# Performance work log

Hardware: AMD Instinct MI355X
Metric: run time of the kernel (lower is better)

Reference implementation:

```python
import jax, jax.numpy as jnp
import numpy as np

N_NODES = 100000
N_EDGES = 3200000
IN_DIM = 256
HID = 64


def setup_inputs() -> dict:
    key = jax.random.key(0)
    ks = jax.random.split(key, 8)
    x = jax.random.normal(ks[0], (N_NODES, IN_DIM), dtype=jnp.float32)
    edge_index = jax.random.randint(ks[1], (2, N_EDGES), 0, N_NODES, dtype=jnp.int32)
    s = lambda k, shp, fan_in: jax.random.normal(k, shp, dtype=jnp.float32) / np.sqrt(fan_in)
    return {
        "x": x,
        "edge_index": edge_index,
        "W1": s(ks[2], (IN_DIM, HID), IN_DIM),
        "b1": jnp.zeros((HID,), jnp.float32),
        "W2": s(ks[3], (HID, HID), HID),
        "b2": jnp.zeros((HID,), jnp.float32),
        "Wl1": s(ks[4], (2 * HID, HID), 2 * HID),
        "bl1": jnp.zeros((HID,), jnp.float32),
        "Wl2": s(ks[5], (HID, 1), HID),
        "bl2": jnp.zeros((1,), jnp.float32),
    }


def gcn_conv(h, src, dst, W, b, n_nodes):
    # PyG GCNConv: linear transform, add self-loops, symmetric norm, scatter-add
    h = h @ W  # [N, out]
    loop = jnp.arange(n_nodes, dtype=src.dtype)
    src_f = jnp.concatenate([src, loop])
    dst_f = jnp.concatenate([dst, loop])
    deg = jax.ops.segment_sum(jnp.ones_like(dst_f, dtype=h.dtype), dst_f,
                              num_segments=n_nodes)
    dinv = jnp.where(deg > 0, jax.lax.rsqrt(jnp.maximum(deg, 1e-12)), 0.0)
    norm = dinv[src_f] * dinv[dst_f]  # [E+N]
    msg = h[src_f] * norm[:, None]     # gather + scale
    out = jax.ops.segment_sum(msg, dst_f, num_segments=n_nodes)
    return out + b


def reference(x, edge_index, W1, b1, W2, b2, Wl1, bl1, Wl2, bl2):
    n = x.shape[0]
    src, dst = edge_index[0], edge_index[1]
    # encode (inference: dropout is identity)
    h = gcn_conv(x, src, dst, W1, b1, n)
    h = jax.nn.relu(h)
    z = gcn_conv(h, src, dst, W2, b2, n)
    # decode: gather src/dst embeddings, concat, MLP, sigmoid
    ef = jnp.concatenate([z[src], z[dst]], axis=1)  # [E, 2*HID]
    e = jax.nn.relu(ef @ Wl1 + bl1)
    e = e @ Wl2 + bl2
    return jax.nn.sigmoid(e)
```

## Files before the change

kernel.cpp:

```cpp
#include <hip/hip_runtime.h>
#include <hip/hip_bf16.h>
#include <math.h>

#define HID 64
#define IN_DIM 256
#define NPB 400
#define NB  250
#define CAP 14336
#define TILE 8192
#define NW  64
#define NKEY (NPB * NW)

typedef unsigned short u16;
typedef unsigned int u32;

using bf16x8 = __attribute__((ext_vector_type(8))) short;
using f32x4  = __attribute__((ext_vector_type(4))) float;

__device__ __forceinline__ float bf2f(u16 v) {
    return __uint_as_float((u32)v << 16);
}
__device__ __forceinline__ u16 f2bf(float f) {
    __hip_bfloat16 b = __float2bfloat16(f);
    return *(u16*)&b;
}

__global__ __launch_bounds__(256) void binit(int* __restrict__ bcur) {
    int b = threadIdx.x + blockIdx.x * 256;
    if (b < NB) bcur[b] = b * CAP;
}

__global__ __launch_bounds__(256) void bucket_fill(const int* __restrict__ src,
                                                   const int* __restrict__ dst,
                                                   int* __restrict__ bcur,
                                                   int2* __restrict__ bpair, int E) {
    __shared__ int hist[NB], cnt2[NB], gbase[NB];
    int tid = threadIdx.x;
    int base = blockIdx.x * TILE;
    for (int i = tid; i < NB; i += 256) { hist[i] = 0; cnt2[i] = 0; }
    __syncthreads();
    for (int i = 0; i < TILE / 256; ++i) {
        int e = base + i * 256 + tid;
        if (e < E) atomicAdd(&hist[dst[e] / NPB], 1);
    }
    __syncthreads();
    for (int b = tid; b < NB; b += 256)
        if (hist[b]) gbase[b] = atomicAdd(&bcur[b], hist[b]);
    __syncthreads();
    for (int i = 0; i < TILE / 256; ++i) {
        int e = base + i * 256 + tid;
        if (e < E) {
            int d = dst[e];
            int b = d / NPB;
            int lp = atomicAdd(&cnt2[b], 1);
            bpair[gbase[b] + lp] = make_int2(src[e], ((d - b * NPB) << 22) | e);
        }
    }
}

__global__ __launch_bounds__(512) void csr_scatter(const int* __restrict__ bcur,
                                                   const int2* __restrict__ bpair,
                                                   int* __restrict__ csr_src,
                                                   int* __restrict__ csr_eid,
                                                   int* __restrict__ noff,
                                                   int* __restrict__ ndeg,
                                                   float* __restrict__ dinv) {
    extern __shared__ int smem[];
    int* cnt  = smem;
    int* tsum = smem + NKEY;
    int* wsum = smem + NKEY + 512;
    int tid = threadIdx.x, b = blockIdx.x;
    int node0 = b * NPB;
    int pbeg = b * CAP;
    int cntE = bcur[b] - pbeg;

    for (int i = tid; i < NKEY; i += 512) cnt[i] = 0;
    __syncthreads();
    for (int i = tid; i < cntE; i += 512) {
        int2 p = bpair[pbeg + i];
        int key = (((p.y >> 22) & 511) << 6) | ((u32)p.x >> 11);
        atomicAdd(&cnt[key], 1);
    }
    __syncthreads();
    {
        int base = tid * (NKEY / 512);
        int s = 0;
#pragma unroll
        for (int j = 0; j < NKEY / 512; ++j) s += cnt[base + j];
        tsum[tid] = s;
    }
    __syncthreads();
    {
        int lane = tid & 63, wid = tid >> 6;
        int v = tsum[tid];
        int incl = v;
#pragma unroll
        for (int s = 1; s < 64; s <<= 1) {
            int t = __shfl_up(incl, s, 64);
            if (lane >= s) incl += t;
        }
        if (lane == 63) wsum[wid] = incl;
        __syncthreads();
        if (tid == 0) {
            int run = 0;
#pragma unroll
            for (int w = 0; w < 8; ++w) { int t = wsum[w]; wsum[w] = run; run += t; }
        }
        __syncthreads();
        tsum[tid] = wsum[wid] + incl - v;
    }
    __syncthreads();
    {
        int base = tid * (NKEY / 512);
        int run = tsum[tid];
#pragma unroll
        for (int j = 0; j < NKEY / 512; ++j) {
            int cv = cnt[base + j];
            cnt[base + j] = run;
            run += cv;
        }
    }
    __syncthreads();
    for (int dl = tid; dl < NPB; dl += 512) {
        int beg = cnt[dl << 6];
        int end = (dl < NPB - 1) ? cnt[(dl + 1) << 6] : cntE;
        noff[node0 + dl] = pbeg + beg;
        ndeg[node0 + dl] = end - beg;
        dinv[node0 + dl] = rsqrtf((float)(end - beg) + 1.0f);
    }
    __syncthreads();
    for (int i = tid; i < cntE; i += 512) {
        int2 p = bpair[pbeg + i];
        int key = (((p.y >> 22) & 511) << 6) | ((u32)p.x >> 11);
        int pos = atomicAdd(&cnt[key], 1);
        csr_src[pbeg + pos] = p.x;
        csr_eid[pbeg + pos] = p.y & 0x3FFFFF;
    }
}

template<int K, int COLS, int MODE>
__global__ __launch_bounds__(256) void mfma_gemm(const float* __restrict__ A,
                                                 const float* __restrict__ W,
                                                 const float* __restrict__ dinv,
                                                 const float* __restrict__ bias,
                                                 u16* __restrict__ out_b,
                                                 float* __restrict__ out_f,
                                                 int N) {
    constexpr int KP = K + 8;
    constexpr int NT = COLS / 16;
    __shared__ __align__(16) u16 Wh[COLS * KP];
    __shared__ __align__(16) u16 Wl[COLS * KP];

    const int tid  = threadIdx.x;
    const int wave = tid >> 6;
    const int lane = tid & 63;
    const int lr   = lane & 15;
    const int kg   = lane >> 4;
    const int row0 = blockIdx.x * 64;

    for (int e = tid; e < K * COLS; e += 256) {
        int k = e / COLS, c = e % COLS;
        int gidx = (MODE == 2) ? (((c >> 6) * K + k) * 64 + (c & 63)) : e;
        float f = W[gidx];
        u16 hi = f2bf(f);
        u16 lo = f2bf(f - bf2f(hi));
        Wh[c * KP + k] = hi;
        Wl[c * KP + k] = lo;
    }
    __syncthreads();

    const int arow = row0 + wave * 16 + lr;
    const float* ar = A + (size_t)(arow < N ? arow : N - 1) * K + kg * 8;

    f32x4 acc[NT];
#pragma unroll
    for (int c = 0; c < NT; ++c) acc[c] = (f32x4){0.f, 0.f, 0.f, 0.f};

#pragma unroll
    for (int ks = 0; ks < K; ks += 32) {
        float4 v0 = *(const float4*)(ar + ks);
        float4 v1 = *(const float4*)(ar + ks + 4);
        bf16x8 ah, al;
        {
            u16 h0 = f2bf(v0.x), h1 = f2bf(v0.y), h2 = f2bf(v0.z), h3 = f2bf(v0.w);
            u16 h4 = f2bf(v1.x), h5 = f2bf(v1.y), h6 = f2bf(v1.z), h7 = f2bf(v1.w);
            ah = (bf16x8){(short)h0, (short)h1, (short)h2, (short)h3,
                          (short)h4, (short)h5, (short)h6, (short)h7};
            al = (bf16x8){(short)f2bf(v0.x - bf2f(h0)), (short)f2bf(v0.y - bf2f(h1)),
                          (short)f2bf(v0.z - bf2f(h2)), (short)f2bf(v0.w - bf2f(h3)),
                          (short)f2bf(v1.x - bf2f(h4)), (short)f2bf(v1.y - bf2f(h5)),
                          (short)f2bf(v1.z - bf2f(h6)), (short)f2bf(v1.w - bf2f(h7))};
        }
#pragma unroll
        for (int c = 0; c < NT; ++c) {
            const int wrow = c * 16 + lr;
            bf16x8 bh = *(const bf16x8*)(Wh + wrow * KP + ks + kg * 8);
            bf16x8 bl = *(const bf16x8*)(Wl + wrow * KP + ks + kg * 8);
            acc[c] = __builtin_amdgcn_mfma_f32_16x16x32_bf16(ah, bh, acc[c], 0, 0, 0);
            acc[c] = __builtin_amdgcn_mfma_f32_16x16x32_bf16(ah, bl, acc[c], 0, 0, 0);
            acc[c] = __builtin_amdgcn_mfma_f32_16x16x32_bf16(al, bh, acc[c], 0, 0, 0);
        }
    }

#pragma unroll
    for (int rr = 0; rr < 4; ++rr) {
        int n = row0 + wave * 16 + kg * 4 + rr;
        if (n >= N) continue;
        float dv = (MODE == 0) ? dinv[n] : 1.f;
#pragma unroll
        for (int c = 0; c < NT; ++c) {
            int col = c * 16 + lr;
            float v = acc[c][rr];
            if (MODE == 0) {
                out_b[(size_t)n * 64 + col] = f2bf(v * dv);
            } else {
                if (col < 64) out_b[(size_t)n * 64 + col] = f2bf(v);
                else out_f[(size_t)n * 64 + (col - 64)] = v + bias[col - 64];
            }
        }
    }
}

__global__ __launch_bounds__(256) void gather_kernel(const int* __restrict__ noff,
                                                     const int* __restrict__ ndeg,
                                                     const int* __restrict__ csr_src,
                                                     const u16* __restrict__ ts,
                                                     const float* __restrict__ dinv,
                                                     const float* __restrict__ bias,
                                                     float* __restrict__ outh, int N,
                                                     int do_relu) {
    long tid = (long)blockIdx.x * blockDim.x + threadIdx.x;
    int v = (int)(tid >> 6), j = (int)(tid & 63);
    if (v >= N) return;
    int l = j & 7, g = j >> 3;
    const uint4* tp = (const uint4*)ts;
    float a0 = 0.f, a1 = 0.f, a2 = 0.f, a3 = 0.f;
    float a4 = 0.f, a5 = 0.f, a6 = 0.f, a7 = 0.f;
    int beg = noff[v], end = beg + ndeg[v];

#define ACCUM(U)                              \
    a0 += __uint_as_float((U).x << 16);       \
    a1 += __uint_as_float((U).x & 0xffff0000u); \
    a2 += __uint_as_float((U).y << 16);       \
    a3 += __uint_as_float((U).y & 0xffff0000u); \
    a4 += __uint_as_float((U).z << 16);       \
    a5 += __uint_as_float((U).z & 0xffff0000u); \
    a6 += __uint_as_float((U).w << 16);       \
    a7 += __uint_as_float((U).w & 0xffff0000u);

    int k = beg + g;
    while (k + 24 < end) {
        int s0 = csr_src[k];
        int s1 = csr_src[k + 8];
        int s2 = csr_src[k + 16];
        int s3 = csr_src[k + 24];
        uint4 u0 = tp[((u32)s0 << 3) + l];
        uint4 u1 = tp[((u32)s1 << 3) + l];
        uint4 u2 = tp[((u32)s2 << 3) + l];
        uint4 u3 = tp[((u32)s3 << 3) + l];
        ACCUM(u0); ACCUM(u1); ACCUM(u2); ACCUM(u3);
        k += 32;
    }
    while (k < end) {
        int s = csr_src[k];
        uint4 u = tp[((u32)s << 3) + l];
        ACCUM(u);
        k += 8;
    }
#pragma unroll
    for (int o = 8; o < 64; o <<= 1) {
        a0 += __shfl_xor(a0, o, 64);
        a1 += __shfl_xor(a1, o, 64);
        a2 += __shfl_xor(a2, o, 64);
        a3 += __shfl_xor(a3, o, 64);
        a4 += __shfl_xor(a4, o, 64);
        a5 += __shfl_xor(a5, o, 64);
        a6 += __shfl_xor(a6, o, 64);
        a7 += __shfl_xor(a7, o, 64);
    }
    uint4 su = tp[((u32)v << 3) + l];
    ACCUM(su);
#undef ACCUM
    float dv = dinv[v];
    const float* bp = bias + 8 * l;
    float4 b4a = *(const float4*)(bp);
    float4 b4b = *(const float4*)(bp + 4);
    float4 r0, r1;
    r0.x = a0 * dv + b4a.x; r0.y = a1 * dv + b4a.y;
    r0.z = a2 * dv + b4a.z; r0.w = a3 * dv + b4a.w;
    r1.x = a4 * dv + b4b.x; r1.y = a5 * dv + b4b.y;
    r1.z = a6 * dv + b4b.z; r1.w = a7 * dv + b4b.w;
    if (do_relu) {
        r0.x = fmaxf(r0.x, 0.f); r0.y = fmaxf(r0.y, 0.f);
        r0.z = fmaxf(r0.z, 0.f); r0.w = fmaxf(r0.w, 0.f);
        r1.x = fmaxf(r1.x, 0.f); r1.y = fmaxf(r1.y, 0.f);
        r1.z = fmaxf(r1.z, 0.f); r1.w = fmaxf(r1.w, 0.f);
    }
    if (g == 0) {
        float* op = outh + ((u32)v << 6) + 8 * l;
        *(float4*)(op) = r0;
        *(float4*)(op + 4) = r1;
    }
}

__global__ __launch_bounds__(256) void decode_kernel(const int* __restrict__ noff,
                                                     const int* __restrict__ ndeg,
                                                     const int* __restrict__ csr_src,
                                                     const int* __restrict__ csr_eid,
                                                     const u16* __restrict__ a,
                                                     const float* __restrict__ c,
                                                     const float* __restrict__ Wl2,
                                                     const float* __restrict__ bl2,
                                                     float* __restrict__ out, int N) {
    long tid = (long)blockIdx.x * blockDim.x + threadIdx.x;
    int v = (int)(tid >> 6), j = (int)(tid & 63);
    if (v >= N) return;
    int l = j & 7, g = j >> 3;
    const float* cv = c + ((u32)v << 6) + 8 * l;
    float4 ca = *(const float4*)(cv);
    float4 cb = *(const float4*)(cv + 4);
    const float* wv = Wl2 + 8 * l;
    float4 wa = *(const float4*)(wv);
    float4 wb = *(const float4*)(wv + 4);
    float bl2v = bl2[0];
    const uint4* ap = (const uint4*)a;
    int beg = noff[v], end = beg + ndeg[v];

#define EDGEP(U, P)                                                   \
    {                                                                 \
        float f0 = __uint_as_float((U).x << 16);                      \
        float f1 = __uint_as_float((U).x & 0xffff0000u);              \
        float f2 = __uint_as_float((U).y << 16);                      \
        float f3 = __uint_as_float((U).y & 0xffff0000u);              \
        float f4 = __uint_as_float((U).z << 16);                      \
        float f5 = __uint_as_float((U).z & 0xffff0000u);              \
        float f6 = __uint_as_float((U).w << 16);                      \
        float f7 = __uint_as_float((U).w & 0xffff0000u);              \
        P  = fmaxf(f0 + ca.x, 0.f) * wa.x;                            \
        P += fmaxf(f1 + ca.y, 0.f) * wa.y;                            \
        P += fmaxf(f2 + ca.z, 0.f) * wa.z;                            \
        P += fmaxf(f3 + ca.w, 0.f) * wa.w;                            \
        P += fmaxf(f4 + cb.x, 0.f) * wb.x;                            \
        P += fmaxf(f5 + cb.y, 0.f) * wb.y;                            \
        P += fmaxf(f6 + cb.z, 0.f) * wb.z;                            \
        P += fmaxf(f7 + cb.w, 0.f) * wb.w;                            \
    }

    int k = beg + g;
    while (k + 8 < end) {
        int s0 = csr_src[k];
        int s1 = csr_src[k + 8];
        int e0 = csr_eid[k];
        int e1 = csr_eid[k + 8];
        uint4 u0 = ap[((u32)s0 << 3) + l];
        uint4 u1 = ap[((u32)s1 << 3) + l];
        float p0, p1;
        EDGEP(u0, p0);
        EDGEP(u1, p1);
        p0 += __shfl_xor(p0, 1, 64);
        p1 += __shfl_xor(p1, 1, 64);
        p0 += __shfl_xor(p0, 2, 64);
        p1 += __shfl_xor(p1, 2, 64);
        p0 += __shfl_xor(p0, 4, 64);
        p1 += __shfl_xor(p1, 4, 64);
        if (l == 0) {
            out[e0] = __builtin_amdgcn_rcpf(1.f + __expf(-(p0 + bl2v)));
            out[e1] = __builtin_amdgcn_rcpf(1.f + __expf(-(p1 + bl2v)));
        }
        k += 16;
    }
    if (k < end) {
        int s0 = csr_src[k];
        int e0 = csr_eid[k];
        uint4 u0 = ap[((u32)s0 << 3) + l];
        float p0;
        EDGEP(u0, p0);
        p0 += __shfl_xor(p0, 1, 64);
        p0 += __shfl_xor(p0, 2, 64);
        p0 += __shfl_xor(p0, 4, 64);
        if (l == 0) out[e0] = __builtin_amdgcn_rcpf(1.f + __expf(-(p0 + bl2v)));
    }
#undef EDGEP
}

extern "C" void kernel_launch(void* const* d_in, const int* in_sizes, int n_in,
                              void* d_out, int out_size, void* d_ws, size_t ws_size,
                              hipStream_t stream) {
    const float* x   = (const float*)d_in[0];
    const int*   ei  = (const int*)d_in[1];
    const float* W1  = (const float*)d_in[2];
    const float* b1  = (const float*)d_in[3];
    const float* W2  = (const float*)d_in[4];
    const float* b2  = (const float*)d_in[5];
    const float* Wl1 = (const float*)d_in[6];
    const float* bl1 = (const float*)d_in[7];
    const float* Wl2 = (const float*)d_in[8];
    const float* bl2 = (const float*)d_in[9];
    float* out = (float*)d_out;

    const int N = in_sizes[0] / IN_DIM;
    const int E = in_sizes[1] / 2;
    const int* src = ei;
    const int* dst = ei + E;

    char* ws = (char*)d_ws;
    float* dinv    = (float*)ws;  ws += (size_t)(N + 64) * 4;
    int*   noff    = (int*)ws;    ws += (size_t)(N + 64) * 4;
    int*   ndeg    = (int*)ws;    ws += (size_t)(N + 64) * 4;
    int*   bcur    = (int*)ws;    ws += 1024;
    int*   csr_src = (int*)ws;    ws += (size_t)NB * CAP * 4;
    int*   csr_eid = (int*)ws;    ws += (size_t)NB * CAP * 4;
    u16*   tb      = (u16*)ws;    ws += (size_t)N * HID * 2;
    float* h       = (float*)ws;  ws += (size_t)N * HID * 4;
    float* c       = (float*)ws;  ws += (size_t)N * HID * 4;
    int2*  bpair   = (int2*)h;

    const int TPB = 256;
    long nodeT = (long)N * HID;
    int nodeBlocks = (int)((nodeT + TPB - 1) / TPB);
    int tBlocks = (E + TILE - 1) / TILE;
    int gBlocks = (N + 63) / 64;
    size_t sortBytes = (size_t)(NKEY + 512 + 8) * sizeof(int);

    binit<<<1, TPB, 0, stream>>>(bcur);
    bucket_fill<<<tBlocks, TPB, 0, stream>>>(src, dst, bcur, bpair, E);
    csr_scatter<<<NB, 512, sortBytes, stream>>>(bcur, bpair, csr_src, csr_eid,
                                                noff, ndeg, dinv);

    mfma_gemm<IN_DIM, 64, 0><<<gBlocks, TPB, 0, stream>>>(x, W1, dinv, nullptr, tb, nullptr, N);
    gather_kernel<<<nodeBlocks, TPB, 0, stream>>>(noff, ndeg, csr_src, tb, dinv, b1, h, N, 1);

    mfma_gemm<HID, 64, 0><<<gBlocks, TPB, 0, stream>>>(h, W2, dinv, nullptr, tb, nullptr, N);
    gather_kernel<<<nodeBlocks, TPB, 0, stream>>>(noff, ndeg, csr_src, tb, dinv, b2, h, N, 0);

    mfma_gemm<HID, 128, 2><<<gBlocks, TPB, 0, stream>>>(h, Wl1, nullptr, bl1, tb, c, N);

    decode_kernel<<<nodeBlocks, TPB, 0, stream>>>(noff, ndeg, csr_src, csr_eid, tb, c, Wl2, bl2, out, N);
}
```

Before: 423.8 us.

## Bucket decode outputs by edge id and scatter through LDS for coalesced writes

The decode kernel no longer writes each sigmoid output straight to a random edge position. Results are staged as (edge id, value) pairs in LDS and binned into edge-id buckets with atomics, then a new oscatter kernel assembles each bucket in shared memory and writes it out with coalesced float4 stores. Each block now handles 16 nodes per wave, so there are fewer blocks. This removes uncoalesced 4-byte scattered stores to the output, at the cost of an extra kernel pass, 8-byte pair traffic, LDS/global atomics, and reuse of the h buffer as pair storage.

```diff
diff --git a/kernel.cpp b/kernel.cpp
--- a/kernel.cpp
+++ b/kernel.cpp
@@ -10,6 +10,8 @@
 #define TILE 8192
 #define NW  64
 #define NKEY (NPB * NW)
+#define OEB 12800
+#define LCAP 2560
 
 typedef unsigned short u16;
 typedef unsigned int u32;
@@ -25,9 +27,13 @@
     return *(u16*)&b;
 }
 
-__global__ __launch_bounds__(256) void binit(int* __restrict__ bcur) {
+__global__ __launch_bounds__(256) void binit(int* __restrict__ bcur,
+                                             int* __restrict__ ocur) {
     int b = threadIdx.x + blockIdx.x * 256;
-    if (b < NB) bcur[b] = b * CAP;
+    if (b < NB) {
+        bcur[b] = b * CAP;
+        ocur[b] = b * OEB;
+    }
 }
 
 __global__ __launch_bounds__(256) void bucket_fill(const int* __restrict__ src,
@@ -311,20 +317,37 @@
                                                      const float* __restrict__ c,
                                                      const float* __restrict__ Wl2,
                                                      const float* __restrict__ bl2,
-                                                     float* __restrict__ out, int N) {
-    long tid = (long)blockIdx.x * blockDim.x + threadIdx.x;
-    int v = (int)(tid >> 6), j = (int)(tid & 63);
-    if (v >= N) return;
+                                                     int2* __restrict__ opair,
+                                                     int* __restrict__ ocur, int N) {
+    __shared__ int2 lbuf[LCAP];
+    __shared__ int lhist[NB];
+    __shared__ int lgb[NB];
+    __shared__ int lcnt;
+    int tid = threadIdx.x;
+    for (int i = tid; i < NB; i += 256) lhist[i] = 0;
+    if (tid == 0) lcnt = 0;
+    __syncthreads();
+
+    int wave = tid >> 6, j = tid & 63;
     int l = j & 7, g = j >> 3;
-    const float* cv = c + ((u32)v << 6) + 8 * l;
-    float4 ca = *(const float4*)(cv);
-    float4 cb = *(const float4*)(cv + 4);
     const float* wv = Wl2 + 8 * l;
     float4 wa = *(const float4*)(wv);
     float4 wb = *(const float4*)(wv + 4);
     float bl2v = bl2[0];
     const uint4* ap = (const uint4*)a;
-    int beg = noff[v], end = beg + ndeg[v];
+    int node0 = blockIdx.x * 64 + wave * 16;
+
+#define EMIT(EID, VAL)                                                       \
+    {                                                                        \
+        int idx_ = atomicAdd(&lcnt, 1);                                      \
+        if (idx_ < LCAP) {                                                   \
+            lbuf[idx_] = make_int2((EID), __float_as_int(VAL));              \
+            atomicAdd(&lhist[(EID) / OEB], 1);                               \
+        } else {                                                             \
+            int pos_ = atomicAdd(&ocur[(EID) / OEB], 1);                     \
+            opair[pos_] = make_int2((EID), __float_as_int(VAL));             \
+        }                                                                    \
+    }
 
 #define EDGEP(U, P)                                                   \
     {                                                                 \
@@ -346,41 +369,89 @@
         P += fmaxf(f7 + cb.w, 0.f) * wb.w;                            \
     }
 
-    int k = beg + g;
-    while (k + 8 < end) {
-        int s0 = csr_src[k];
-        int s1 = csr_src[k + 8];
-        int e0 = csr_eid[k];
-        int e1 = csr_eid[k + 8];
-        uint4 u0 = ap[((u32)s0 << 3) + l];
-        uint4 u1 = ap[((u32)s1 << 3) + l];
-        float p0, p1;
-        EDGEP(u0, p0);
-        EDGEP(u1, p1);
-        p0 += __shfl_xor(p0, 1, 64);
-        p1 += __shfl_xor(p1, 1, 64);
-        p0 += __shfl_xor(p0, 2, 64);
-        p1 += __shfl_xor(p1, 2, 64);
-        p0 += __shfl_xor(p0, 4, 64);
-        p1 += __shfl_xor(p1, 4, 64);
-        if (l == 0) {
-            out[e0] = __builtin_amdgcn_rcpf(1.f + __expf(-(p0 + bl2v)));
-            out[e1] = __builtin_amdgcn_rcpf(1.f + __expf(-(p1 + bl2v)));
-        }
-        k += 16;
-    }
-    if (k < end) {
-        int s0 = csr_src[k];
-        int e0 = csr_eid[k];
-        uint4 u0 = ap[((u32)s0 << 3) + l];
-        float p0;
-        EDGEP(u0, p0);
-        p0 += __shfl_xor(p0, 1, 64);
-        p0 += __shfl_xor(p0, 2, 64);
-        p0 += __shfl_xor(p0, 4, 64);
-        if (l == 0) out[e0] = __builtin_amdgcn_rcpf(1.f + __expf(-(p0 + bl2v)));
+    for (int ni = 0; ni < 16; ++ni) {
+        int v = node0 + ni;
+        if (v >= N) break;
+        const float* cv = c + ((u32)v << 6) + 8 * l;
+        float4 ca = *(const float4*)(cv);
+        float4 cb = *(const float4*)(cv + 4);
+        int beg = noff[v], end = beg + ndeg[v];
+
+        int k = beg + g;
+        while (k + 8 < end) {
+            int s0 = csr_src[k];
+            int s1 = csr_src[k + 8];
+            int e0 = csr_eid[k];
+            int e1 = csr_eid[k + 8];
+            uint4 u0 = ap[((u32)s0 << 3) + l];
+            uint4 u1 = ap[((u32)s1 << 3) + l];
+            float p0, p1;
+            EDGEP(u0, p0);
+            EDGEP(u1, p1);
+            p0 += __shfl_xor(p0, 1, 64);
+            p1 += __shfl_xor(p1, 1, 64);
+            p0 += __shfl_xor(p0, 2, 64);
+            p1 += __shfl_xor(p1, 2, 64);
+            p0 += __shfl_xor(p0, 4, 64);
+            p1 += __shfl_xor(p1, 4, 64);
+            if (l == 0) {
+                float v0 = __builtin_amdgcn_rcpf(1.f + __expf(-(p0 + bl2v)));
+                float v1 = __builtin_amdgcn_rcpf(1.f + __expf(-(p1 + bl2v)));
+                EMIT(e0, v0);
+                EMIT(e1, v1);
+            }
+            k += 16;
+        }
+        if (k < end) {
+            int s0 = csr_src[k];
+            int e0 = csr_eid[k];
+            uint4 u0 = ap[((u32)s0 << 3) + l];
+            float p0;
+            EDGEP(u0, p0);
+            p0 += __shfl_xor(p0, 1, 64);
+            p0 += __shfl_xor(p0, 2, 64);
+            p0 += __shfl_xor(p0, 4, 64);
+            if (l == 0) {
+                float v0 = __builtin_amdgcn_rcpf(1.f + __expf(-(p0 + bl2v)));
+                EMIT(e0, v0);
+            }
+        }
     }
 #undef EDGEP
+#undef EMIT
+    __syncthreads();
+
+    for (int b = tid; b < NB; b += 256) {
+        int hcount = lhist[b];
+        if (hcount) lgb[b] = atomicAdd(&ocur[b], hcount);
+    }
+    __syncthreads();
+    int total = lcnt < LCAP ? lcnt : LCAP;
+    for (int i = tid; i < total; i += 256) {
+        int2 p = lbuf[i];
+        int ob = p.x / OEB;
+        int pos = atomicAdd(&lgb[ob], 1);
+        opair[pos] = p;
+    }
+}
+
+__global__ __launch_bounds__(256) void oscatter(const int2* __restrict__ opair,
+                                                float* __restrict__ out, int E) {
+    __shared__ float lval[OEB];
+    int tid = threadIdx.x, b = blockIdx.x;
+    int base = b * OEB;
+    int n = E - base;
+    if (n > OEB) n = OEB;
+    for (int i = tid; i < n; i += 256) {
+        int2 p = opair[base + i];
+        lval[p.x - base] = __int_as_float(p.y);
+    }
+    __syncthreads();
+    int n4 = n >> 2;
+    float4* out4 = (float4*)(out + base);
+    const float4* lv4 = (const float4*)lval;
+    for (int i = tid; i < n4; i += 256) out4[i] = lv4[i];
+    for (int i = (n4 << 2) + tid; i < n; i += 256) out[base + i] = lval[i];
 }
 
 extern "C" void kernel_launch(void* const* d_in, const int* in_sizes, int n_in,
@@ -408,21 +479,25 @@
     int*   noff    = (int*)ws;    ws += (size_t)(N + 64) * 4;
     int*   ndeg    = (int*)ws;    ws += (size_t)(N + 64) * 4;
     int*   bcur    = (int*)ws;    ws += 1024;
+    int*   ocur    = (int*)ws;    ws += 1024;
     int*   csr_src = (int*)ws;    ws += (size_t)NB * CAP * 4;
     int*   csr_eid = (int*)ws;    ws += (size_t)NB * CAP * 4;
     u16*   tb      = (u16*)ws;    ws += (size_t)N * HID * 2;
     float* h       = (float*)ws;  ws += (size_t)N * HID * 4;
     float* c       = (float*)ws;  ws += (size_t)N * HID * 4;
     int2*  bpair   = (int2*)h;
+    int2*  opair   = (int2*)h;
 
     const int TPB = 256;
     long nodeT = (long)N * HID;
     int nodeBlocks = (int)((nodeT + TPB - 1) / TPB);
     int tBlocks = (E + TILE - 1) / TILE;
     int gBlocks = (N + 63) / 64;
+    int dBlocks = (N + 63) / 64;
+    int oBlocks = (E + OEB - 1) / OEB;
     size_t sortBytes = (size_t)(NKEY + 512 + 8) * sizeof(int);
 
-    binit<<<1, TPB, 0, stream>>>(bcur);
+    binit<<<1, TPB, 0, stream>>>(bcur, ocur);
     bucket_fill<<<tBlocks, TPB, 0, stream>>>(src, dst, bcur, bpair, E);
     csr_scatter<<<NB, 512, sortBytes, stream>>>(bcur, bpair, csr_src, csr_eid,
                                                 noff, ndeg, dinv);
@@ -435,5 +510,7 @@
 
     mfma_gemm<HID, 128, 2><<<gBlocks, TPB, 0, stream>>>(h, Wl1, nullptr, bl1, tb, c, N);
 
-    decode_kernel<<<nodeBlocks, TPB, 0, stream>>>(noff, ndeg, csr_src, csr_eid, tb, c, Wl2, bl2, out, N);
-}
+    decode_kernel<<<dBlocks, TPB, 0, stream>>>(noff, ndeg, csr_src, csr_eid, tb, c,
+                                               Wl2, bl2, opair, ocur, N);
+    oscatter<<<oBlocks, TPB, 0, stream>>>(opair, out, E);
+}
```

After: 424.7 us. About the same (+0.2%).
